# Kernel tuning notes

Measured on AMD Instinct MI355X. Metric: run time of the kernel, lower is better.

## Reference

```python
import jax, jax.numpy as jnp
import numpy as np

K = 20
EPS = 1e-5  # BatchNorm eps; eval mode with running_mean=0, running_var=1


def _lrelu(x):
    return jnp.where(x >= 0, x, 0.2 * x)


def _bn(x, g, b):
    # eval-mode BN (fresh running stats: mean=0, var=1); channel axis = 1
    shape = (1, -1) + (1,) * (x.ndim - 2)
    return x * (g / jnp.sqrt(1.0 + EPS)).reshape(shape) + b.reshape(shape)


def _knn_idx(x, k):
    # x: (B, C, N). Negative squared euclidean distance, top-k = nearest.
    xx = jnp.sum(x * x, axis=1)                      # (B, N)
    inner = jnp.einsum('bcn,bcm->bnm', x, x)         # (B, N, N)
    neg_d = 2.0 * inner - xx[:, :, None] - xx[:, None, :]
    return jax.lax.top_k(neg_d, k)[1]                # (B, N, K)


def _gather(x, idx):
    # x: (B, C, N), idx: (B, N, K) -> (B, C, N, K)
    return jax.vmap(lambda xb, ib: xb[:, ib])(x, idx)


def setup_inputs() -> dict:
    key = jax.random.key(0)
    ks = jax.random.split(key, 32)
    B, N = 8, 2048
    d = {}
    d['x'] = jax.random.normal(ks[0], (B, 3, N), jnp.float32)

    def w(k_, o, i):
        return jax.random.normal(k_, (o, i), jnp.float32) * (1.0 / np.sqrt(i))

    d['W1'] = w(ks[1], 64, 3)
    d['W2'] = w(ks[2], 64, 64)
    d['W3'] = w(ks[3], 128, 64)
    d['W4'] = w(ks[4], 256, 128)
    d['W5'] = w(ks[5], 1024, 512)
    bn_dims = [64, 64, 128, 256, 1024, 512, 256]
    for i, c in enumerate(bn_dims):
        d[f'g{i+1}'] = 1.0 + 0.1 * jax.random.normal(ks[6 + 2 * i], (c,), jnp.float32)
        d[f'b{i+1}'] = 0.1 * jax.random.normal(ks[7 + 2 * i], (c,), jnp.float32)
    d['L1W'] = w(ks[20], 512, 2048)
    d['L2W'] = w(ks[21], 256, 512)
    d['L2b'] = 0.1 * jax.random.normal(ks[22], (256,), jnp.float32)
    d['L3W'] = w(ks[23], 40, 256)
    d['L3b'] = 0.1 * jax.random.normal(ks[24], (40,), jnp.float32)
    return d


def reference(x, W1, W2, W3, W4, W5,
              g1, b1, g2, b2, g3, b3, g4, b4, g5, b5, g6, b6, g7, b7,
              L1W, L2W, L2b, L3W, L3b):
    idx = _knn_idx(x, K)  # shared neighbor indices for all EdgeConv blocks

    h = _lrelu(_bn(jnp.einsum('oc,bcnk->bonk', W1, _gather(x, idx)), g1, b1))
    x1 = h.max(axis=-1)                               # (B, 64, N)
    h = _lrelu(_bn(jnp.einsum('oc,bcnk->bonk', W2, _gather(x1, idx)), g2, b2))
    x2 = h.max(axis=-1)                               # (B, 64, N)
    h = _lrelu(_bn(jnp.einsum('oc,bcnk->bonk', W3, _gather(x2, idx)), g3, b3))
    x3 = h.max(axis=-1)                               # (B, 128, N)
    h = _lrelu(_bn(jnp.einsum('oc,bcnk->bonk', W4, _gather(x3, idx)), g4, b4))
    x4 = h.max(axis=-1)                               # (B, 256, N)

    cat = jnp.concatenate([x1, x2, x3, x4], axis=1)   # (B, 512, N)
    h = _lrelu(_bn(jnp.einsum('oc,bcn->bon', W5, cat), g5, b5))  # (B, 1024, N)

    f = jnp.concatenate([h.max(axis=-1), h.mean(axis=-1)], axis=1)  # (B, 2048)
    f = _lrelu(_bn(f @ L1W.T, g6, b6))
    f = _lrelu(_bn(f @ L2W.T + L2b, g7, b7))          # dropout is identity in eval
    return f @ L3W.T + L3b                            # (B, 40)
```

## Files before the change

kernel.cpp:

```cpp
#include <hip/hip_runtime.h>
#include <math.h>


#define WS_IDX      0
#define WS_Y16      1310720
#define WS_XCAT16   9699328
#define WS_W16      26476544
#define WS_FMAX     27615232
#define WS_FSUM     27648000
#define WS_A1       27680768
#define WS_A2       27697152

typedef _Float16 f16x8 __attribute__((ext_vector_type(8)));
typedef float f32x4 __attribute__((ext_vector_type(4)));

struct F3 { float x, y, z; };

__device__ __forceinline__ float lrelu(float v) { return (v >= 0.f) ? v : 0.2f * v; }
__device__ __forceinline__ unsigned sortable_f32(float f) {
  unsigned b = __float_as_uint(f);
  return b ^ (((unsigned)((int)b >> 31)) | 0x80000000u);
}
__device__ __forceinline__ float desort_f32(unsigned u) {
  unsigned b = (u & 0x80000000u) ? (u ^ 0x80000000u) : ~u;
  return __uint_as_float(b);
}

__global__ __launch_bounds__(256) void knn_prep_kernel(
    const float* __restrict__ x, const float* __restrict__ W1,
    const float* __restrict__ g1, const float* __restrict__ b1,
    const float* __restrict__ W2, const float* __restrict__ W3,
    const float* __restrict__ W4, const float* __restrict__ W5,
    _Float16* __restrict__ w16, unsigned* __restrict__ fzero,
    int* __restrict__ idxo, _Float16* __restrict__ xcat) {
  __shared__ F3 pts_s[2048];
  __shared__ unsigned long long cand_s[8][60];
  __shared__ unsigned cnt_s[8];
  __shared__ int sel_s[8][20];
  int tid = threadIdx.x;

  if (blockIdx.x >= 2048) {
    int bid = blockIdx.x - 2048;
#pragma unroll
    for (int t = 0; t < 8; ++t) {
      int i = bid * 2048 + t * 256 + tid;
      if (i < 4096) w16[i] = (_Float16)W2[i];
      else if (i < 12288) w16[i] = (_Float16)W3[i - 4096];
      else if (i < 45056) w16[i] = (_Float16)W4[i - 12288];
      else if (i < 569344) w16[i] = (_Float16)W5[i - 45056];
      else fzero[i - 569344] = 0u;
    }
    return;
  }

  int lwave = tid >> 6, lane = tid & 63;
  int qbase = blockIdx.x * 8;
  int b = qbase >> 11;
  int nbase = qbase & 2047;
  const float* xb = x + b * 6144;
#pragma unroll
  for (int i = 0; i < 8; ++i) {
    int m = tid + i * 256;
    F3 p; p.x = xb[m]; p.y = xb[2048 + m]; p.z = xb[4096 + m];
    pts_s[m] = p;
  }
  if (lane == 0) cnt_s[lwave * 2] = 0, cnt_s[lwave * 2 + 1] = 0;
  __syncthreads();

  F3 q[2];
  float qw[2];
  unsigned lmax[2] = {0u, 0u};
#pragma unroll
  for (int qi = 0; qi < 2; ++qi) {
    q[qi] = pts_s[nbase + lwave * 2 + qi];
    qw[qi] = q[qi].x * q[qi].x + q[qi].y * q[qi].y + q[qi].z * q[qi].z;
  }
  for (int j = 0; j < 32; ++j) {
    F3 p = pts_s[j * 64 + lane];
    float pw = p.x * p.x + p.y * p.y + p.z * p.z;
#pragma unroll
    for (int qi = 0; qi < 2; ++qi) {
      float nd = 2.0f * (q[qi].x * p.x + q[qi].y * p.y + q[qi].z * p.z) -
                 qw[qi] - pw;
      unsigned key = sortable_f32(nd);
      lmax[qi] = (key > lmax[qi]) ? key : lmax[qi];
    }
  }
  unsigned lo[2] = {0u, 0u}, hi[2] = {0x8001u, 0x8001u};
  for (int it = 0; it < 16; ++it) {
#pragma unroll
    for (int qi = 0; qi < 2; ++qi) {
      unsigned mid = (lo[qi] + hi[qi] + 1) >> 1;
      int cnt = __popcll(__ballot(lmax[qi] >= (mid << 16)));
      if (cnt >= 20) lo[qi] = mid; else hi[qi] = mid;
    }
  }
  unsigned T[2] = {lo[0] << 16, lo[1] << 16};
  for (int j = 0; j < 32; ++j) {
    int m = j * 64 + lane;
    F3 p = pts_s[m];
    float pw = p.x * p.x + p.y * p.y + p.z * p.z;
#pragma unroll
    for (int qi = 0; qi < 2; ++qi) {
      float nd = 2.0f * (q[qi].x * p.x + q[qi].y * p.y + q[qi].z * p.z) -
                 qw[qi] - pw;
      unsigned key = sortable_f32(nd);
      if (key >= T[qi]) {
        unsigned pos = atomicAdd(&cnt_s[lwave * 2 + qi], 1u);
        if (pos < 60)
          cand_s[lwave * 2 + qi][pos] =
              (((unsigned long long)key) << 32) | (unsigned)(2047 - m);
      }
    }
  }
#pragma unroll
  for (int qi = 0; qi < 2; ++qi) {
    int qq = lwave * 2 + qi;
    int row = qbase + qq;
    int outb = row * 20;
    unsigned C = cnt_s[qq];
    if (C <= 60) {
      unsigned long long v = (lane < (int)C) ? ~cand_s[qq][lane] : ~0ull;
#pragma unroll
      for (int k = 2; k <= 64; k <<= 1) {
#pragma unroll
        for (int jj = k >> 1; jj > 0; jj >>= 1) {
          unsigned long long o = __shfl_xor(v, jj, 64);
          bool lower = (lane & jj) == 0;
          bool up = (lane & k) == 0;
          bool takeMin = (lower == up);
          bool sw = takeMin ? (o < v) : (o > v);
          v = sw ? o : v;
        }
      }
      if (lane < 20) {
        unsigned long long pack = ~v;
        int m = 2047 - (int)(pack & 0xFFFFFFFFu);
        idxo[outb + lane] = m;
        sel_s[qq][lane] = m;
      }
    } else {
      unsigned long long prev = ~0ull;
      for (int r = 0; r < 20; ++r) {
        unsigned long long best = 0ull;
        for (int j = 0; j < 32; ++j) {
          int m = j * 64 + lane;
          F3 p = pts_s[m];
          float pw = p.x * p.x + p.y * p.y + p.z * p.z;
          float nd = 2.0f * (q[qi].x * p.x + q[qi].y * p.y + q[qi].z * p.z) -
                     qw[qi] - pw;
          unsigned long long pk =
              (((unsigned long long)sortable_f32(nd)) << 32) |
              (unsigned)(2047 - m);
          bool ok = (pk < prev) & (pk > best);
          best = ok ? pk : best;
        }
#pragma unroll
        for (int off = 1; off < 64; off <<= 1) {
          unsigned long long o = __shfl_xor(best, off, 64);
          best = (o > best) ? o : best;
        }
        int m = 2047 - (int)(best & 0xFFFFFFFFu);
        if (lane == 0) { idxo[outb + r] = m; sel_s[qq][r] = m; }
        prev = best;
      }
    }
  }
  float w0 = W1[lane * 3 + 0], w1 = W1[lane * 3 + 1], w2 = W1[lane * 3 + 2];
  float inv = 1.0f / sqrtf(1.0f + 1e-5f);
  float sc = g1[lane] * inv, bi = b1[lane];
#pragma unroll
  for (int qi = 0; qi < 2; ++qi) {
    int qq = lwave * 2 + qi;
    int row = qbase + qq;
    float mx = -3.4e38f, mn = 3.4e38f;
#pragma unroll
    for (int k = 0; k < 20; ++k) {
      F3 p = pts_s[sel_s[qq][k]];
      float v = w0 * p.x + w1 * p.y + w2 * p.z;
      mx = fmaxf(mx, v);
      mn = fminf(mn, v);
    }
    float v = (sc >= 0.0f) ? mx : mn;
    xcat[row * 512 + lane] = (_Float16)lrelu(sc * v + bi);
  }
}

template <int C, int COFF>
__global__ __launch_bounds__(256) void gmax_kernel(const _Float16* __restrict__ y,
                                                   const int* __restrict__ idx,
                                                   const float* __restrict__ g,
                                                   const float* __restrict__ bb,
                                                   _Float16* __restrict__ xcat) {
  constexpr int TP = C / 8;
  int e = blockIdx.x * 256 + threadIdx.x;
  int c8 = e & (TP - 1);
  int pg = e / TP;
  int b = pg >> 11;
  const int* ix = idx + pg * 20;
  int mm[20];
#pragma unroll
  for (int k = 0; k < 20; ++k) mm[k] = ix[k];
  int base = b * 2048 * C + c8 * 8;
  float mx[8], mn[8];
#pragma unroll
  for (int i = 0; i < 8; ++i) { mx[i] = -3.4e38f; mn[i] = 3.4e38f; }
#pragma unroll
  for (int k = 0; k < 20; ++k) {
    f16x8 v = *(const f16x8*)&y[base + mm[k] * C];
#pragma unroll
    for (int i = 0; i < 8; ++i) {
      float f = (float)v[i];
      mx[i] = fmaxf(mx[i], f);
      mn[i] = fminf(mn[i], f);
    }
  }
  float inv = 1.0f / sqrtf(1.0f + 1e-5f);
  f16x8 outv;
#pragma unroll
  for (int i = 0; i < 8; ++i) {
    float s = g[c8 * 8 + i] * inv;
    float v = (s >= 0.0f) ? mx[i] : mn[i];
    outv[i] = (_Float16)lrelu(s * v + bb[c8 * 8 + i]);
  }
  *(f16x8*)&xcat[pg * 512 + COFF + c8 * 8] = outv;
}

template <int CIN, int COUT, int XOFF>
__global__ __launch_bounds__(256) void gemm_mfma(const _Float16* __restrict__ Wh,
                                                 const _Float16* __restrict__ Xc,
                                                 _Float16* __restrict__ Y) {
  constexpr int BN = (COUT < 128) ? COUT : 128;
  constexpr int MT = (BN == 128) ? 4 : 2;
  __shared__ _Float16 Xs[128 * 40];
  __shared__ _Float16 Ws[BN * 40];
  int tid = threadIdx.x;
  int lane = tid & 63, w = tid >> 6;
  int wm = (BN == 128) ? (w & 1) : w;
  int wn = (BN == 128) ? (w >> 1) : 0;
  int col = lane & 15, quad = lane >> 4;
  int pg0 = blockIdx.x * 128;
  int o0 = blockIdx.y * BN;
  int r0 = tid >> 2;
  int c8 = (tid & 3) * 8;
  f32x4 acc[MT][4] = {};
  for (int k0 = 0; k0 < CIN; k0 += 32) {
    f16x8 xa = *(const f16x8*)&Xc[(pg0 + r0) * 512 + XOFF + k0 + c8];
    f16x8 xb2 = *(const f16x8*)&Xc[(pg0 + r0 + 64) * 512 + XOFF + k0 + c8];
    f16x8 wa = *(const f16x8*)&Wh[(o0 + r0) * CIN + k0 + c8];
    f16x8 wb;
    if (BN == 128) wb = *(const f16x8*)&Wh[(o0 + r0 + 64) * CIN + k0 + c8];
    __syncthreads();
    *(f16x8*)&Xs[r0 * 40 + c8] = xa;
    *(f16x8*)&Xs[(r0 + 64) * 40 + c8] = xb2;
    *(f16x8*)&Ws[r0 * 40 + c8] = wa;
    if (BN == 128) *(f16x8*)&Ws[(r0 + 64) * 40 + c8] = wb;
    __syncthreads();
    f16x8 af[MT], bf[4];
#pragma unroll
    for (int t = 0; t < MT; ++t)
      af[t] = *(const f16x8*)&Xs[(wm * (MT * 16) + t * 16 + col) * 40 + quad * 8];
#pragma unroll
    for (int t = 0; t < 4; ++t)
      bf[t] = *(const f16x8*)&Ws[(wn * 64 + t * 16 + col) * 40 + quad * 8];
#pragma unroll
    for (int mt = 0; mt < MT; ++mt)
#pragma unroll
      for (int nt = 0; nt < 4; ++nt)
        acc[mt][nt] = __builtin_amdgcn_mfma_f32_16x16x32_f16(af[mt], bf[nt],
                                                             acc[mt][nt], 0, 0, 0);
  }
#pragma unroll
  for (int mt = 0; mt < MT; ++mt)
#pragma unroll
    for (int nt = 0; nt < 4; ++nt)
#pragma unroll
      for (int r = 0; r < 4; ++r) {
        int p = pg0 + wm * (MT * 16) + mt * 16 + quad * 4 + r;
        int ch = o0 + wn * 64 + nt * 16 + col;
        Y[p * COUT + ch] = (_Float16)acc[mt][nt][r];
      }
}

__global__ __launch_bounds__(256) void gemm5_kernel(
    const _Float16* __restrict__ Wh, const _Float16* __restrict__ Xc,
    const float* __restrict__ g5, const float* __restrict__ b5,
    unsigned* __restrict__ fmax, float* __restrict__ fsum) {
  __shared__ _Float16 Xs[128 * 40];
  __shared__ _Float16 Ws[128 * 40];
  __shared__ float pm[256], ps[256];
  int tid = threadIdx.x;
  int lane = tid & 63, w = tid >> 6;
  int wm = w & 1, wn = w >> 1;
  int col = lane & 15, quad = lane >> 4;
  int pg0 = blockIdx.x * 128;
  int o0 = blockIdx.y * 128;
  int r0 = tid >> 2;
  int c8 = (tid & 3) * 8;

  f32x4 acc[4][4] = {};
  for (int k0 = 0; k0 < 512; k0 += 32) {
    f16x8 xa = *(const f16x8*)&Xc[(pg0 + r0) * 512 + k0 + c8];
    f16x8 xb = *(const f16x8*)&Xc[(pg0 + r0 + 64) * 512 + k0 + c8];
    f16x8 wa = *(const f16x8*)&Wh[(o0 + r0) * 512 + k0 + c8];
    f16x8 wb = *(const f16x8*)&Wh[(o0 + r0 + 64) * 512 + k0 + c8];
    __syncthreads();
    *(f16x8*)&Xs[r0 * 40 + c8] = xa;
    *(f16x8*)&Xs[(r0 + 64) * 40 + c8] = xb;
    *(f16x8*)&Ws[r0 * 40 + c8] = wa;
    *(f16x8*)&Ws[(r0 + 64) * 40 + c8] = wb;
    __syncthreads();
    f16x8 af[4], bf[4];
#pragma unroll
    for (int t = 0; t < 4; ++t) {
      af[t] = *(const f16x8*)&Xs[(wm * 64 + t * 16 + col) * 40 + quad * 8];
      bf[t] = *(const f16x8*)&Ws[(wn * 64 + t * 16 + col) * 40 + quad * 8];
    }
#pragma unroll
    for (int mt = 0; mt < 4; ++mt)
#pragma unroll
      for (int nt = 0; nt < 4; ++nt)
        acc[mt][nt] = __builtin_amdgcn_mfma_f32_16x16x32_f16(af[mt], bf[nt],
                                                             acc[mt][nt], 0, 0, 0);
  }
  float inv = 1.0f / sqrtf(1.0f + 1e-5f);
#pragma unroll
  for (int nt = 0; nt < 4; ++nt) {
    int o = o0 + wn * 64 + nt * 16 + col;
    float sc = g5[o] * inv, bi = b5[o];
    float mx = -3.4e38f, sm = 0.f;
#pragma unroll
    for (int mt = 0; mt < 4; ++mt)
#pragma unroll
      for (int r = 0; r < 4; ++r) {
        float v = lrelu(acc[mt][nt][r] * sc + bi);
        mx = fmaxf(mx, v);
        sm += v;
      }
    mx = fmaxf(mx, __shfl_xor(mx, 16, 64));
    sm += __shfl_xor(sm, 16, 64);
    mx = fmaxf(mx, __shfl_xor(mx, 32, 64));
    sm += __shfl_xor(sm, 32, 64);
    if (quad == 0) {
      pm[wm * 128 + wn * 64 + nt * 16 + col] = mx;
      ps[wm * 128 + wn * 64 + nt * 16 + col] = sm;
    }
  }
  __syncthreads();
  if (tid < 128) {
    float m = fmaxf(pm[tid], pm[128 + tid]);
    float s = ps[tid] + ps[128 + tid];
    int b = pg0 >> 11;
    atomicMax(&fmax[b * 1024 + o0 + tid], sortable_f32(m));
    atomicAdd(&fsum[b * 1024 + o0 + tid], s);
  }
}

__global__ __launch_bounds__(256) void l1_kernel(const unsigned* __restrict__ fmax,
                                                 const float* __restrict__ fsum,
                                                 const float* __restrict__ L1W,
                                                 const float* __restrict__ g6,
                                                 const float* __restrict__ b6,
                                                 float* __restrict__ a1) {
  int gw = (blockIdx.x * 256 + threadIdx.x) >> 6;
  int lane = threadIdx.x & 63;
  int b = gw >> 9, o = gw & 511;
  float s = 0.f;
#pragma unroll
  for (int i = 0; i < 32; ++i) {
    int j = lane + i * 64;
    float fj = (j < 1024) ? desort_f32(fmax[b * 1024 + j])
                          : fsum[b * 1024 + j - 1024] * (1.0f / 2048.0f);
    s += fj * L1W[o * 2048 + j];
  }
#pragma unroll
  for (int off = 1; off < 64; off <<= 1) s += __shfl_xor(s, off, 64);
  if (lane == 0) {
    float scv = g6[o] / sqrtf(1.0f + 1e-5f);
    a1[b * 512 + o] = lrelu(s * scv + b6[o]);
  }
}

__global__ __launch_bounds__(256) void l2_kernel(const float* __restrict__ a1,
                                                 const float* __restrict__ L2W,
                                                 const float* __restrict__ L2b,
                                                 const float* __restrict__ g7,
                                                 const float* __restrict__ b7,
                                                 float* __restrict__ a2) {
  int gw = (blockIdx.x * 256 + threadIdx.x) >> 6;
  int lane = threadIdx.x & 63;
  int b = gw >> 8, o = gw & 255;
  float s = 0.f;
#pragma unroll
  for (int i = 0; i < 8; ++i) {
    int j = lane + i * 64;
    s += a1[b * 512 + j] * L2W[o * 512 + j];
  }
#pragma unroll
  for (int off = 1; off < 64; off <<= 1) s += __shfl_xor(s, off, 64);
  if (lane == 0) {
    float v = s + L2b[o];
    float scv = g7[o] / sqrtf(1.0f + 1e-5f);
    a2[b * 256 + o] = lrelu(v * scv + b7[o]);
  }
}

__global__ __launch_bounds__(256) void l3_kernel(const float* __restrict__ a2,
                                                 const float* __restrict__ L3W,
                                                 const float* __restrict__ L3b,
                                                 float* __restrict__ out) {
  int gw = (blockIdx.x * 256 + threadIdx.x) >> 6;
  int lane = threadIdx.x & 63;
  int b = gw / 40, o = gw % 40;
  float s = 0.f;
#pragma unroll
  for (int i = 0; i < 4; ++i) {
    int j = lane + i * 64;
    s += a2[b * 256 + j] * L3W[o * 256 + j];
  }
#pragma unroll
  for (int off = 1; off < 64; off <<= 1) s += __shfl_xor(s, off, 64);
  if (lane == 0) out[b * 40 + o] = s + L3b[o];
}

extern "C" void kernel_launch(void* const* d_in, const int* in_sizes, int n_in,
                              void* d_out, int out_size, void* d_ws, size_t ws_size,
                              hipStream_t stream) {
  const float* x = (const float*)d_in[0];
  const float* W1 = (const float*)d_in[1];
  const float* W2 = (const float*)d_in[2];
  const float* W3 = (const float*)d_in[3];
  const float* W4 = (const float*)d_in[4];
  const float* W5 = (const float*)d_in[5];
  const float* g1 = (const float*)d_in[6];  const float* b1 = (const float*)d_in[7];
  const float* g2 = (const float*)d_in[8];  const float* b2 = (const float*)d_in[9];
  const float* g3 = (const float*)d_in[10]; const float* b3 = (const float*)d_in[11];
  const float* g4 = (const float*)d_in[12]; const float* b4 = (const float*)d_in[13];
  const float* g5 = (const float*)d_in[14]; const float* b5 = (const float*)d_in[15];
  const float* g6 = (const float*)d_in[16]; const float* b6 = (const float*)d_in[17];
  const float* g7 = (const float*)d_in[18]; const float* b7 = (const float*)d_in[19];
  const float* L1W = (const float*)d_in[20];
  const float* L2W = (const float*)d_in[21];
  const float* L2b = (const float*)d_in[22];
  const float* L3W = (const float*)d_in[23];
  const float* L3b = (const float*)d_in[24];

  char* w = (char*)d_ws;
  int* idxb = (int*)(w + WS_IDX);
  _Float16* y16 = (_Float16*)(w + WS_Y16);
  _Float16* xcat16 = (_Float16*)(w + WS_XCAT16);
  _Float16* w16 = (_Float16*)(w + WS_W16);
  unsigned* fmax = (unsigned*)(w + WS_FMAX);
  float* fsum = (float*)(w + WS_FSUM);
  float* a1 = (float*)(w + WS_A1);
  float* a2 = (float*)(w + WS_A2);

  knn_prep_kernel<<<2334, 256, 0, stream>>>(x, W1, g1, b1, W2, W3, W4, W5,
                                            w16, fmax, idxb, xcat16);
  gemm_mfma<64, 64, 0><<<dim3(128, 1), 256, 0, stream>>>(w16, xcat16, y16);
  gmax_kernel<64, 64><<<512, 256, 0, stream>>>(y16, idxb, g2, b2, xcat16);
  gemm_mfma<64, 128, 64><<<dim3(128, 1), 256, 0, stream>>>(w16 + 4096, xcat16, y16);
  gmax_kernel<128, 128><<<1024, 256, 0, stream>>>(y16, idxb, g3, b3, xcat16);
  gemm_mfma<128, 256, 128><<<dim3(128, 2), 256, 0, stream>>>(w16 + 12288, xcat16, y16);
  gmax_kernel<256, 256><<<2048, 256, 0, stream>>>(y16, idxb, g4, b4, xcat16);
  gemm5_kernel<<<dim3(128, 8), 256, 0, stream>>>(w16 + 45056, xcat16, g5, b5, fmax, fsum);
  l1_kernel<<<1024, 256, 0, stream>>>(fmax, fsum, L1W, g6, b6, a1);
  l2_kernel<<<512, 256, 0, stream>>>(a1, L2W, L2b, g7, b7, a2);
  l3_kernel<<<80, 256, 0, stream>>>(a2, L3W, L3b, (float*)d_out);
}
```

Baseline: 235.2 us.

## Rewrite final conv GEMM with 256x256 tiles and async global-to-LDS double buffering

Replaces the 128x128-tile gemm5 kernel with a 512-thread, 256x256-tile kernel. It stages K-tiles of 64 directly from global memory into swizzled, double-buffered LDS using global_load_lds and overlaps the next tile's loads with the MFMAs through fine-grained waitcnt, barriers and setprio. The per-block LDS reduction is dropped in favour of per-wave atomics on the max and sum buffers. The aim is to cut redundant global traffic and load latency on the largest GEMM, at the cost of 128KB of LDS per block and only 256 blocks, which may limit occupancy and leave some CUs idle.

```diff
diff --git a/kernel.cpp b/kernel.cpp
--- a/kernel.cpp
+++ b/kernel.cpp
@@ -282,58 +282,121 @@
       }
 }
 
-__global__ __launch_bounds__(256) void gemm5_kernel(
+typedef const __attribute__((address_space(1))) void* gas1_t;
+typedef __attribute__((address_space(3))) void* las3_t;
+
+__device__ __forceinline__ void stage16(const _Float16* g, char* l) {
+  __builtin_amdgcn_global_load_lds((gas1_t)g, (las3_t)l, 16, 0, 0);
+}
+
+__global__ __launch_bounds__(512, 2) void gemm5_kernel(
     const _Float16* __restrict__ Wh, const _Float16* __restrict__ Xc,
     const float* __restrict__ g5, const float* __restrict__ b5,
     unsigned* __restrict__ fmax, float* __restrict__ fsum) {
-  __shared__ _Float16 Xs[128 * 40];
-  __shared__ _Float16 Ws[128 * 40];
-  __shared__ float pm[256], ps[256];
-  int tid = threadIdx.x;
-  int lane = tid & 63, w = tid >> 6;
-  int wm = w & 1, wn = w >> 1;
-  int col = lane & 15, quad = lane >> 4;
-  int pg0 = blockIdx.x * 128;
-  int o0 = blockIdx.y * 128;
-  int r0 = tid >> 2;
-  int c8 = (tid & 3) * 8;
-
-  f32x4 acc[4][4] = {};
-  for (int k0 = 0; k0 < 512; k0 += 32) {
-    f16x8 xa = *(const f16x8*)&Xc[(pg0 + r0) * 512 + k0 + c8];
-    f16x8 xb = *(const f16x8*)&Xc[(pg0 + r0 + 64) * 512 + k0 + c8];
-    f16x8 wa = *(const f16x8*)&Wh[(o0 + r0) * 512 + k0 + c8];
-    f16x8 wb = *(const f16x8*)&Wh[(o0 + r0 + 64) * 512 + k0 + c8];
-    __syncthreads();
-    *(f16x8*)&Xs[r0 * 40 + c8] = xa;
-    *(f16x8*)&Xs[(r0 + 64) * 40 + c8] = xb;
-    *(f16x8*)&Ws[r0 * 40 + c8] = wa;
-    *(f16x8*)&Ws[(r0 + 64) * 40 + c8] = wb;
-    __syncthreads();
-    f16x8 af[4], bf[4];
-#pragma unroll
-    for (int t = 0; t < 4; ++t) {
-      af[t] = *(const f16x8*)&Xs[(wm * 64 + t * 16 + col) * 40 + quad * 8];
-      bf[t] = *(const f16x8*)&Ws[(wn * 64 + t * 16 + col) * 40 + quad * 8];
-    }
-#pragma unroll
-    for (int mt = 0; mt < 4; ++mt)
-#pragma unroll
-      for (int nt = 0; nt < 4; ++nt)
-        acc[mt][nt] = __builtin_amdgcn_mfma_f32_16x16x32_f16(af[mt], bf[nt],
-                                                             acc[mt][nt], 0, 0, 0);
-  }
-  float inv = 1.0f / sqrtf(1.0f + 1e-5f);
-#pragma unroll
-  for (int nt = 0; nt < 4; ++nt) {
-    int o = o0 + wn * 64 + nt * 16 + col;
-    float sc = g5[o] * inv, bi = b5[o];
+  __shared__ __attribute__((aligned(16))) char lds[131072];
+  char* ldsc = (char*)lds;
+  const int tid = threadIdx.x;
+  const int lane = tid & 63, w = tid >> 6;
+  const int wm = w & 1, wn = w >> 1;
+  const int col = lane & 15, quad = lane >> 4;
+  const int pg0 = blockIdx.x * 256;
+  const int o0 = blockIdx.y * 256;
+
+  const int so = tid << 4;
+  const int sl = so ^ (((so >> 9) & 3) << 5);
+  const int srow0 = sl >> 7;
+  const int skc0 = (sl & 127) >> 1;
+
+#define STG(srcp, baserow, ktile, regoff, i)                                  \
+  stage16((srcp) + ((baserow) + (i) * 64 + srow0) * 512 + (ktile) * 64 + skc0,\
+          ldsc + (regoff) + (i) * 8192 + (w << 10))
+
+  const int swc = ((col >> 2) & 3) << 5;
+  const int labA = (col * 128 + quad * 16) ^ swc;
+  const int labB = ((wn & 1) * 8192 + col * 128 + quad * 16) ^ swc;
+
+#define RDA(m, kk) (*(const f16x8*)(rA + ((labA ^ ((kk) << 6)) + (m) * 2048)))
+#define RDB(n, kk) (*(const f16x8*)(rB + ((labB ^ ((kk) << 6)) + (n) * 2048)))
+
+  f32x4 acc[8][4] = {};
+
+  STG(Wh, o0, 0, 32768, 0);       STG(Wh, o0, 0, 32768, 1);
+  STG(Wh, o0 + 128, 0, 49152, 0); STG(Wh, o0 + 128, 0, 49152, 1);
+  STG(Xc, pg0, 0, 0, 0);          STG(Xc, pg0 + 128, 0, 16384, 0);
+  STG(Xc, pg0, 0, 0, 1);          STG(Xc, pg0 + 128, 0, 16384, 1);
+  asm volatile("s_waitcnt vmcnt(0)" ::: "memory");
+  __builtin_amdgcn_s_barrier();
+
+  for (int t = 0; t < 8; ++t) {
+    const int nt = t + 1;
+    const char* rA = ldsc + (t & 1) * 65536 + wm * 16384;
+    const char* rB = ldsc + (t & 1) * 65536 + 32768 + (wn >> 1) * 16384;
+    const int nreg = (nt & 1) * 65536;
+    f16x8 bf[4][2];
+#pragma unroll
+    for (int p = 0; p < 4; ++p) {
+      f16x8 a[2][2];
+#pragma unroll
+      for (int mm = 0; mm < 2; ++mm)
+#pragma unroll
+        for (int kk = 0; kk < 2; ++kk)
+          a[mm][kk] = RDA(2 * p + mm, kk);
+      if (p == 0) {
+#pragma unroll
+        for (int n = 0; n < 4; ++n)
+#pragma unroll
+          for (int kk = 0; kk < 2; ++kk)
+            bf[n][kk] = RDB(n, kk);
+      }
+      if (t < 7) {
+        if (p == 0) { STG(Wh, o0, nt, nreg + 32768, 0);
+                      STG(Wh, o0, nt, nreg + 32768, 1); }
+        if (p == 1) { STG(Wh, o0 + 128, nt, nreg + 49152, 0);
+                      STG(Wh, o0 + 128, nt, nreg + 49152, 1); }
+        if (p == 2) { STG(Xc, pg0, nt, nreg + 0, 0);
+                      STG(Xc, pg0 + 128, nt, nreg + 16384, 0); }
+        if (p == 3) { STG(Xc, pg0, nt, nreg + 0, 1);
+                      STG(Xc, pg0 + 128, nt, nreg + 16384, 1); }
+      }
+      if (p == 1) {
+        if (t < 7) { asm volatile("s_waitcnt vmcnt(4)" ::: "memory"); }
+        else       { asm volatile("s_waitcnt vmcnt(0)" ::: "memory"); }
+      }
+      if (p == 3 && t < 7) {
+        asm volatile("s_waitcnt vmcnt(2)" ::: "memory");
+      }
+      __builtin_amdgcn_s_barrier();
+      asm volatile("s_waitcnt lgkmcnt(0)" ::: "memory");
+      __builtin_amdgcn_sched_barrier(0);
+      __builtin_amdgcn_s_setprio(1);
+#pragma unroll
+      for (int mm = 0; mm < 2; ++mm)
+#pragma unroll
+        for (int n = 0; n < 4; ++n)
+#pragma unroll
+          for (int kk = 0; kk < 2; ++kk)
+            acc[2 * p + mm][n] = __builtin_amdgcn_mfma_f32_16x16x32_f16(
+                a[mm][kk], bf[n][kk], acc[2 * p + mm][n], 0, 0, 0);
+      __builtin_amdgcn_s_setprio(0);
+      __builtin_amdgcn_s_barrier();
+    }
+  }
+#undef STG
+#undef RDA
+#undef RDB
+
+  const float inv = 1.0f / sqrtf(1.0f + 1e-5f);
+  const int b = pg0 >> 11;
+#pragma unroll
+  for (int n = 0; n < 4; ++n) {
+    int ch = o0 + wn * 64 + n * 16 + col;
+    float sc = g5[ch] * inv, bi = b5[ch];
     float mx = -3.4e38f, sm = 0.f;
 #pragma unroll
-    for (int mt = 0; mt < 4; ++mt)
+    for (int m = 0; m < 8; ++m)
 #pragma unroll
       for (int r = 0; r < 4; ++r) {
-        float v = lrelu(acc[mt][nt][r] * sc + bi);
+        float v = lrelu(acc[m][n][r] * sc + bi);
         mx = fmaxf(mx, v);
         sm += v;
       }
@@ -342,17 +405,9 @@
     mx = fmaxf(mx, __shfl_xor(mx, 32, 64));
     sm += __shfl_xor(sm, 32, 64);
     if (quad == 0) {
-      pm[wm * 128 + wn * 64 + nt * 16 + col] = mx;
-      ps[wm * 128 + wn * 64 + nt * 16 + col] = sm;
-    }
-  }
-  __syncthreads();
-  if (tid < 128) {
-    float m = fmaxf(pm[tid], pm[128 + tid]);
-    float s = ps[tid] + ps[128 + tid];
-    int b = pg0 >> 11;
-    atomicMax(&fmax[b * 1024 + o0 + tid], sortable_f32(m));
-    atomicAdd(&fsum[b * 1024 + o0 + tid], s);
+      atomicMax(&fmax[b * 1024 + ch], sortable_f32(mx));
+      atomicAdd(&fsum[b * 1024 + ch], sm);
+    }
   }
 }
 
@@ -463,7 +518,7 @@
   gmax_kernel<128, 128><<<1024, 256, 0, stream>>>(y16, idxb, g3, b3, xcat16);
   gemm_mfma<128, 256, 128><<<dim3(128, 2), 256, 0, stream>>>(w16 + 12288, xcat16, y16);
   gmax_kernel<256, 256><<<2048, 256, 0, stream>>>(y16, idxb, g4, b4, xcat16);
-  gemm5_kernel<<<dim3(128, 8), 256, 0, stream>>>(w16 + 45056, xcat16, g5, b5, fmax, fsum);
+  gemm5_kernel<<<dim3(64, 4), 512, 0, stream>>>(w16 + 45056, xcat16, g5, b5, fmax, fsum);
   l1_kernel<<<1024, 256, 0, stream>>>(fmax, fsum, L1W, g6, b6, a1);
   l2_kernel<<<512, 256, 0, stream>>>(a1, L2W, L2b, g7, b7, a2);
   l3_kernel<<<80, 256, 0, stream>>>(a2, L3W, L3b, (float*)d_out);
```

Result: faster. 225.0 us (-4.4%).
